# Optimization experiments

Hardware: AMD Instinct MI355X
Metric: run time of the kernel (lower is better)

The kernel has to match this reference:

```python
import jax, jax.numpy as jnp
import numpy as np

N_NODES = 100000
N_EDGES = 1600000
D_FEAT = 64
NUM_LAYERS = 4  # -> num_gcn_layers = 3


def spmm(edge_row, edge_col, edge_vals, x, n_nodes):
    # out[r] = sum_{e: row[e]==r} vals[e] * x[col[e]]
    gathered = edge_vals[:, None] * x[edge_col]  # [E, d]
    return jax.ops.segment_sum(gathered, edge_row, num_segments=n_nodes)


def setup_inputs() -> dict:
    key = jax.random.key(0)
    k1, k2, k3, k4 = jax.random.split(key, 4)
    x = jax.random.normal(k1, (N_NODES, D_FEAT), dtype=jnp.float32)
    edge_row = jax.random.randint(k2, (N_EDGES,), 0, N_NODES, dtype=jnp.int32)
    edge_col = jax.random.randint(k3, (N_EDGES,), 0, N_NODES, dtype=jnp.int32)
    edge_vals = jax.random.uniform(k4, (N_EDGES,), dtype=jnp.float32)
    return {"x": x, "edge_row": edge_row, "edge_col": edge_col, "edge_vals": edge_vals}


def reference(x, edge_row, edge_col, edge_vals):
    # resSumGCN: h_{i+1} = A h_i ; return sum_{i=1..L} h_i
    num_gcn_layers = NUM_LAYERS - 1
    h = x
    acc = jnp.zeros_like(x)
    for _ in range(num_gcn_layers):  # small fixed layer count
        h = spmm(edge_row, edge_col, edge_vals, h, N_NODES)
        acc = acc + h
    return acc
```

## Files before the change

kernel.cpp:

```cpp
#include <hip/hip_runtime.h>

#define N_NODES 100000
#define N_EDGES 1600000
#define D_FEAT  64

#define RSHIFT 8
#define RPB    256
#define NBK    ((N_NODES + RPB - 1) / RPB)
#define CAP    5120
#define EPB    4096
#define KBLK   ((N_EDGES + EPB - 1) / EPB)
#define OROW   (NBK + 1)
#define CVB    ((N_NODES * D_FEAT / 4 + 1023) / 1024)

typedef float f32x2 __attribute__((ext_vector_type(2)));

__device__ __forceinline__ unsigned short f2bf(float f) {
  union { float f; unsigned int i; } v; v.f = f;
  unsigned int b = v.i;
  return (unsigned short)((b + 0x7FFFu + ((b >> 16) & 1u)) >> 16);
}
__device__ __forceinline__ float ulo(int u) { return __int_as_float(u << 16); }
__device__ __forceinline__ float uhi(int u) { return __int_as_float(u & 0xFFFF0000); }
__device__ __forceinline__ f32x2 upk(int u) {
  f32x2 r; r.x = ulo(u); r.y = uhi(u); return r;
}
__device__ __forceinline__ int pk(float a, float b) {
  return (int)f2bf(a) | ((int)f2bf(b) << 16);
}

__global__ __launch_bounds__(1024) void convert_bin(
    const float4* __restrict__ xin, ushort4* __restrict__ xout,
    const int* __restrict__ erow, const int* __restrict__ ecol,
    const float* __restrict__ evals, int2* __restrict__ tmp,
    int* __restrict__ offs) {
  __shared__ int hist[NBK];
  __shared__ int sc[NBK];
  int t = threadIdx.x;
  int k = blockIdx.x;
  if (k >= KBLK) {
    int i = (k - KBLK) * 1024 + t;
    if (i < N_NODES * D_FEAT / 4) {
      float4 v = xin[i];
      ushort4 o;
      o.x = f2bf(v.x); o.y = f2bf(v.y); o.z = f2bf(v.z); o.w = f2bf(v.w);
      xout[i] = o;
    }
    return;
  }
  if (t < NBK) hist[t] = 0;
  __syncthreads();
  int base = k * EPB;
  int nk = N_EDGES - base; if (nk > EPB) nk = EPB;
  int key[4], vb[4], rk[4], bk[4];
#pragma unroll
  for (int j = 0; j < 4; ++j) {
    int li = j * 1024 + t;
    bk[j] = -1;
    if (li < nk) {
      int e = base + li;
      int r = erow[e];
      key[j] = ((r & (RPB - 1)) << 17) | ecol[e];
      vb[j]  = __float_as_int(evals[e]);
      bk[j]  = r >> RSHIFT;
      rk[j]  = atomicAdd(&hist[bk[j]], 1);
    }
  }
  __syncthreads();
  if (t < NBK) sc[t] = hist[t];
  __syncthreads();
  for (int off = 1; off < NBK; off <<= 1) {
    int u = (t >= off && t < NBK) ? sc[t - off] : 0;
    __syncthreads();
    if (t < NBK) sc[t] += u;
    __syncthreads();
  }
  if (t < NBK) {
    int ex = sc[t] - hist[t];
    sc[t] = ex;
    offs[k * OROW + t] = ex;
  }
  if (t == 0) offs[k * OROW + NBK] = nk;
  __syncthreads();
#pragma unroll
  for (int j = 0; j < 4; ++j) {
    if (bk[j] >= 0) {
      int pos = sc[bk[j]] + rk[j];
      tmp[k * EPB + pos] = make_int2(key[j], vb[j]);
    }
  }
}

__global__ __launch_bounds__(512) void build_csr(
    const int2* __restrict__ tmp, const int* __restrict__ offs,
    int2* __restrict__ edges, int* __restrict__ row_beg,
    int* __restrict__ row_end) {
  __shared__ int hist[RPB];
  __shared__ int cur[RPB];
  int b = blockIdx.x;
  int t = threadIdx.x;
  int oct = t >> 3;
  int ol  = t & 7;
  if (t < RPB) hist[t] = 0;
  __syncthreads();
  for (int k = oct; k < KBLK; k += 64) {
    int o0 = offs[k * OROW + b];
    int o1 = offs[k * OROW + b + 1];
    const int2* seg = tmp + k * EPB;
    for (int i = o0 + ol; i < o1; i += 8)
      atomicAdd(&hist[seg[i].x >> 17], 1);
  }
  __syncthreads();
  int v = 0, v2 = 0;
  if (t < RPB) {
    v  = hist[t];
    v2 = (v + 1) & ~1;
    cur[t] = v2;
  }
  __syncthreads();
  for (int off = 1; off < RPB; off <<= 1) {
    int u = (t >= off && t < RPB) ? cur[t - off] : 0;
    __syncthreads();
    if (t < RPB) cur[t] += u;
    __syncthreads();
  }
  int excl2 = 0;
  int base = b * CAP;
  if (t < RPB) {
    excl2 = cur[t] - v2;
    int gr = b * RPB + t;
    if (gr < N_NODES) {
      row_beg[gr] = base + excl2;
      row_end[gr] = base + excl2 + v;
    }
    if (v & 1) edges[base + excl2 + v] = make_int2(0, 0);
  }
  __syncthreads();
  if (t < RPB) cur[t] = excl2;
  __syncthreads();
  for (int k = oct; k < KBLK; k += 64) {
    int o0 = offs[k * OROW + b];
    int o1 = offs[k * OROW + b + 1];
    const int2* seg = tmp + k * EPB;
    for (int i = o0 + ol; i < o1; i += 8) {
      int2 ed = seg[i];
      int pos = atomicAdd(&cur[ed.x >> 17], 1);
      edges[base + pos] = make_int2(ed.x & 0x1FFFF, ed.y);
    }
  }
}

__global__ __launch_bounds__(256) void spmm_oct(
    const int* __restrict__ row_beg, const int* __restrict__ row_end,
    const int2* __restrict__ edges, const int4* __restrict__ xq,
    int4* __restrict__ h_q, float4* __restrict__ out,
    const int4* __restrict__ add1, const int4* __restrict__ add2,
    int final_mode) {
  int t = threadIdx.x;
  int lane = t & 63;
  int oct = lane >> 3;
  int ol  = lane & 7;
  int row = blockIdx.x * 32 + (t >> 6) * 8 + oct;
  int e0 = row_beg[row];
  int e1 = row_end[row];
  const int4* ep = (const int4*)edges + (e0 >> 1);
  int npair = (e1 - e0 + 1) >> 1;
  f32x2 c0 = {0.f, 0.f}, c1 = {0.f, 0.f}, c2 = {0.f, 0.f}, c3 = {0.f, 0.f};

#define GATH(g0, g1, m) \
    g0 = xq[(size_t)(m).x * 8 + ol]; \
    g1 = xq[(size_t)(m).z * 8 + ol];
#define FMA_P(g0, g1, m) { \
    float v0 = __int_as_float((m).y), v1 = __int_as_float((m).w); \
    f32x2 vv0 = {v0, v0}, vv1 = {v1, v1}; \
    c0 += vv0 * upk((g0).x) + vv1 * upk((g1).x); \
    c1 += vv0 * upk((g0).y) + vv1 * upk((g1).y); \
    c2 += vv0 * upk((g0).z) + vv1 * upk((g1).z); \
    c3 += vv0 * upk((g0).w) + vv1 * upk((g1).w); \
  }

  if (npair >= 2) {
    int4 mA0 = ep[0], mA1 = ep[1];
    int4 a0, a1, a2, a3;
    GATH(a0, a1, mA0);
    GATH(a2, a3, mA1);
    int q = 2;
    while (q + 4 <= npair) {
      int4 mB0 = ep[q], mB1 = ep[q + 1];
      int4 b0, b1, b2, b3;
      GATH(b0, b1, mB0);
      GATH(b2, b3, mB1);
      FMA_P(a0, a1, mA0);
      FMA_P(a2, a3, mA1);
      mA0 = ep[q + 2]; mA1 = ep[q + 3];
      GATH(a0, a1, mA0);
      GATH(a2, a3, mA1);
      FMA_P(b0, b1, mB0);
      FMA_P(b2, b3, mB1);
      q += 4;
    }
    if (q + 2 <= npair) {
      int4 mB0 = ep[q], mB1 = ep[q + 1];
      int4 b0, b1, b2, b3;
      GATH(b0, b1, mB0);
      GATH(b2, b3, mB1);
      FMA_P(a0, a1, mA0);
      FMA_P(a2, a3, mA1);
      FMA_P(b0, b1, mB0);
      FMA_P(b2, b3, mB1);
      q += 2;
    } else {
      FMA_P(a0, a1, mA0);
      FMA_P(a2, a3, mA1);
    }
    if (q < npair) {
      int4 m = ep[q];
      int4 g0, g1;
      GATH(g0, g1, m);
      FMA_P(g0, g1, m);
    }
  } else if (npair == 1) {
    int4 m = ep[0];
    int4 g0, g1;
    GATH(g0, g1, m);
    FMA_P(g0, g1, m);
  }
#undef GATH
#undef FMA_P

  size_t oi = (size_t)row * 8 + ol;
  if (final_mode) {
    int4 r1 = add1[oi];
    int4 r2 = add2[oi];
    float4 lo, hi;
    lo.x = c0.x + ulo(r1.x) + ulo(r2.x);
    lo.y = c0.y + uhi(r1.x) + uhi(r2.x);
    lo.z = c1.x + ulo(r1.y) + ulo(r2.y);
    lo.w = c1.y + uhi(r1.y) + uhi(r2.y);
    hi.x = c2.x + ulo(r1.z) + ulo(r2.z);
    hi.y = c2.y + uhi(r1.z) + uhi(r2.z);
    hi.z = c3.x + ulo(r1.w) + ulo(r2.w);
    hi.w = c3.y + uhi(r1.w) + uhi(r2.w);
    out[(size_t)row * 16 + ol * 2]     = lo;
    out[(size_t)row * 16 + ol * 2 + 1] = hi;
  } else {
    int4 pq;
    pq.x = pk(c0.x, c0.y);
    pq.y = pk(c1.x, c1.y);
    pq.z = pk(c2.x, c2.y);
    pq.w = pk(c3.x, c3.y);
    h_q[oi] = pq;
  }
}

extern "C" void kernel_launch(void* const* d_in, const int* in_sizes, int n_in,
                              void* d_out, int out_size, void* d_ws, size_t ws_size,
                              hipStream_t stream) {
  const float* x     = (const float*)d_in[0];
  const int*   erow  = (const int*)d_in[1];
  const int*   ecol  = (const int*)d_in[2];
  const float* evals = (const float*)d_in[3];
  float* out = (float*)d_out;

  const size_t hb_bytes   = (size_t)N_NODES * D_FEAT * 2;
  const size_t ecap_bytes = (size_t)NBK * CAP * sizeof(int2);
  char* ws = (char*)d_ws;
  int4*    xbf  = (int4*)   (ws);
  int4*    bufA = (int4*)   (ws + hb_bytes);
  int2*    tmp  = (int2*)   (ws + hb_bytes);
  int4*    bufB = (int4*)   (ws + 2 * hb_bytes);
  int*     offs = (int*)    (ws + 2 * hb_bytes);
  int2* edges   = (int2*)(ws + 3 * hb_bytes);
  int* row_beg  = (int*) (ws + 3 * hb_bytes + ecap_bytes);
  int* row_end  = (int*) (ws + 3 * hb_bytes + ecap_bytes + 400000);

  const int sblocks = N_NODES / 32;

  convert_bin<<<KBLK + CVB, 1024, 0, stream>>>(
      (const float4*)x, (ushort4*)xbf, erow, ecol, evals, tmp, offs);
  build_csr<<<NBK, 512, 0, stream>>>(tmp, offs, edges, row_beg, row_end);

  spmm_oct<<<sblocks, 256, 0, stream>>>(row_beg, row_end, edges, xbf,
                                        bufA, nullptr, nullptr, nullptr, 0);
  spmm_oct<<<sblocks, 256, 0, stream>>>(row_beg, row_end, edges, bufA,
                                        bufB, nullptr, nullptr, nullptr, 0);
  spmm_oct<<<sblocks, 256, 0, stream>>>(row_beg, row_end, edges, bufB,
                                        nullptr, (float4*)out, bufA, bufB, 1);
}
```

Measured before the change: 228.0 us.

## Sort each row's edges by column and use nontemporal loads/stores in SpMM

Adds a sort_rows kernel that sorts each row's edge list (up to 64 entries) by column index with a wave-level bitonic sort, so gathers within a row hit x in ascending address order. It also switches the SpMM's edge-stream reads, residual reads and output writes to nontemporal loads and stores, keeping those one-touch streams from evicting the gathered feature rows from cache. The extra sort kernel adds a launch and a pass over all edges in exchange for better gather locality across the three SpMM layers.

```diff
diff --git a/kernel.cpp b/kernel.cpp
--- a/kernel.cpp
+++ b/kernel.cpp
@@ -14,6 +14,8 @@
 #define CVB    ((N_NODES * D_FEAT / 4 + 1023) / 1024)
 
 typedef float f32x2 __attribute__((ext_vector_type(2)));
+typedef int   i32x4 __attribute__((ext_vector_type(4)));
+typedef float f32x4 __attribute__((ext_vector_type(4)));
 
 __device__ __forceinline__ unsigned short f2bf(float f) {
   union { float f; unsigned int i; } v; v.f = f;
@@ -27,6 +29,18 @@
 }
 __device__ __forceinline__ int pk(float a, float b) {
   return (int)f2bf(a) | ((int)f2bf(b) << 16);
+}
+__device__ __forceinline__ int4 ntl4(const int4* p) {
+  i32x4 r = __builtin_nontemporal_load((const i32x4*)p);
+  int4 o; o.x = r.x; o.y = r.y; o.z = r.z; o.w = r.w; return o;
+}
+__device__ __forceinline__ void nts4i(int4* p, int4 v) {
+  i32x4 t; t.x = v.x; t.y = v.y; t.z = v.z; t.w = v.w;
+  __builtin_nontemporal_store(t, (i32x4*)p);
+}
+__device__ __forceinline__ void nts4f(float4* p, float4 v) {
+  f32x4 t; t.x = v.x; t.y = v.y; t.z = v.z; t.w = v.w;
+  __builtin_nontemporal_store(t, (f32x4*)p);
 }
 
 __global__ __launch_bounds__(1024) void convert_bin(
@@ -150,6 +164,33 @@
   }
 }
 
+__global__ __launch_bounds__(256) void sort_rows(
+    const int* __restrict__ row_beg, const int* __restrict__ row_end,
+    int2* __restrict__ edges) {
+  int t = threadIdx.x;
+  int lane = t & 63;
+  int w = blockIdx.x * 4 + (t >> 6);
+  int e0 = row_beg[w];
+  int e1 = row_end[w];
+  int len2 = (e1 - e0 + 1) & ~1;
+  if (len2 > 64) return;
+  int k = 0x7FFFFFFF, v = 0;
+  if (lane < len2) { int2 ed = edges[e0 + lane]; k = ed.x; v = ed.y; }
+#pragma unroll
+  for (int size = 2; size <= 64; size <<= 1) {
+#pragma unroll
+    for (int stride = size >> 1; stride >= 1; stride >>= 1) {
+      int ok = __shfl_xor(k, stride);
+      int ov = __shfl_xor(v, stride);
+      bool up    = (lane & size) == 0;
+      bool lower = (lane & stride) == 0;
+      bool takeOther = (lower == up) ? (ok < k) : (ok > k);
+      if (takeOther) { k = ok; v = ov; }
+    }
+  }
+  if (lane < len2) edges[e0 + lane] = make_int2(k, v);
+}
+
 __global__ __launch_bounds__(256) void spmm_oct(
     const int* __restrict__ row_beg, const int* __restrict__ row_end,
     const int2* __restrict__ edges, const int4* __restrict__ xq,
@@ -180,19 +221,19 @@
   }
 
   if (npair >= 2) {
-    int4 mA0 = ep[0], mA1 = ep[1];
+    int4 mA0 = ntl4(ep + 0), mA1 = ntl4(ep + 1);
     int4 a0, a1, a2, a3;
     GATH(a0, a1, mA0);
     GATH(a2, a3, mA1);
     int q = 2;
     while (q + 4 <= npair) {
-      int4 mB0 = ep[q], mB1 = ep[q + 1];
+      int4 mB0 = ntl4(ep + q), mB1 = ntl4(ep + q + 1);
       int4 b0, b1, b2, b3;
       GATH(b0, b1, mB0);
       GATH(b2, b3, mB1);
       FMA_P(a0, a1, mA0);
       FMA_P(a2, a3, mA1);
-      mA0 = ep[q + 2]; mA1 = ep[q + 3];
+      mA0 = ntl4(ep + q + 2); mA1 = ntl4(ep + q + 3);
       GATH(a0, a1, mA0);
       GATH(a2, a3, mA1);
       FMA_P(b0, b1, mB0);
@@ -200,7 +241,7 @@
       q += 4;
     }
     if (q + 2 <= npair) {
-      int4 mB0 = ep[q], mB1 = ep[q + 1];
+      int4 mB0 = ntl4(ep + q), mB1 = ntl4(ep + q + 1);
       int4 b0, b1, b2, b3;
       GATH(b0, b1, mB0);
       GATH(b2, b3, mB1);
@@ -214,13 +255,13 @@
       FMA_P(a2, a3, mA1);
     }
     if (q < npair) {
-      int4 m = ep[q];
+      int4 m = ntl4(ep + q);
       int4 g0, g1;
       GATH(g0, g1, m);
       FMA_P(g0, g1, m);
     }
   } else if (npair == 1) {
-    int4 m = ep[0];
+    int4 m = ntl4(ep + 0);
     int4 g0, g1;
     GATH(g0, g1, m);
     FMA_P(g0, g1, m);
@@ -230,8 +271,8 @@
 
   size_t oi = (size_t)row * 8 + ol;
   if (final_mode) {
-    int4 r1 = add1[oi];
-    int4 r2 = add2[oi];
+    int4 r1 = ntl4(add1 + oi);
+    int4 r2 = ntl4(add2 + oi);
     float4 lo, hi;
     lo.x = c0.x + ulo(r1.x) + ulo(r2.x);
     lo.y = c0.y + uhi(r1.x) + uhi(r2.x);
@@ -241,15 +282,15 @@
     hi.y = c2.y + uhi(r1.z) + uhi(r2.z);
     hi.z = c3.x + ulo(r1.w) + ulo(r2.w);
     hi.w = c3.y + uhi(r1.w) + uhi(r2.w);
-    out[(size_t)row * 16 + ol * 2]     = lo;
-    out[(size_t)row * 16 + ol * 2 + 1] = hi;
+    nts4f(out + (size_t)row * 16 + ol * 2,     lo);
+    nts4f(out + (size_t)row * 16 + ol * 2 + 1, hi);
   } else {
     int4 pq;
     pq.x = pk(c0.x, c0.y);
     pq.y = pk(c1.x, c1.y);
     pq.z = pk(c2.x, c2.y);
     pq.w = pk(c3.x, c3.y);
-    h_q[oi] = pq;
+    nts4i(h_q + oi, pq);
   }
 }
 
@@ -279,6 +320,7 @@
   convert_bin<<<KBLK + CVB, 1024, 0, stream>>>(
       (const float4*)x, (ushort4*)xbf, erow, ecol, evals, tmp, offs);
   build_csr<<<NBK, 512, 0, stream>>>(tmp, offs, edges, row_beg, row_end);
+  sort_rows<<<N_NODES / 4, 256, 0, stream>>>(row_beg, row_end, edges);
 
   spmm_oct<<<sblocks, 256, 0, stream>>>(row_beg, row_end, edges, xbf,
                                         bufA, nullptr, nullptr, nullptr, 0);
```

After: 288.3 us. +26.4%, slower.
